# Performance work log

Hardware: AMD Instinct MI355X
Metric: run time of the kernel (lower is better)

## Reference

```python
import jax, jax.numpy as jnp
import numpy as np

EMBED = 1024
HEADS = 16


def setup_inputs() -> dict:
    key = jax.random.key(0)
    ks = jax.random.split(key, 7)
    scale = 1.0 / np.sqrt(EMBED)
    x = jax.random.normal(ks[0], (4, 2048, EMBED), dtype=jnp.float32)
    Wq = jax.random.normal(ks[1], (EMBED, EMBED), dtype=jnp.float32) * scale
    bq = jax.random.normal(ks[2], (EMBED,), dtype=jnp.float32) * 0.01
    Wk = jax.random.normal(ks[3], (EMBED, EMBED), dtype=jnp.float32) * scale
    bk = jax.random.normal(ks[4], (EMBED,), dtype=jnp.float32) * 0.01
    Wv = jax.random.normal(ks[5], (EMBED, EMBED), dtype=jnp.float32) * scale
    bv = jax.random.normal(ks[6], (EMBED,), dtype=jnp.float32) * 0.01
    return {"x": x, "Wq": Wq, "bq": bq, "Wk": Wk, "bk": bk, "Wv": Wv, "bv": bv}


def reference(x, Wq, bq, Wk, bk, Wv, bv):
    b, s, n = x.shape
    h = HEADS
    d = n // h
    # torch nn.Linear: y = x @ W.T + b
    q = (jnp.einsum("bsn,mn->bsm", x, Wq) + bq).reshape(b, s, h, d).transpose(0, 2, 1, 3)
    k = (jnp.einsum("bsn,mn->bsm", x, Wk) + bk).reshape(b, s, h, d).transpose(0, 2, 1, 3)
    v = (jnp.einsum("bsn,mn->bsm", x, Wv) + bv).reshape(b, s, h, d).transpose(0, 2, 1, 3)
    # scores: [b, h, s_q, s_k]; fixed scale of 1/10 as in the source
    scores = jnp.einsum("bhqd,bhkd->bhqk", q, k) / 10.0
    # NOTE: softmax over dim=-2 (the QUERY axis), matching the source exactly
    attn = jax.nn.softmax(scores, axis=-2)
    out = jnp.einsum("bhqk,bhkd->bhqd", attn, v)
    return out.transpose(0, 2, 1, 3).reshape(b, s, n)
```

## Files before the change

kernel.cpp:

```cpp
#include <hip/hip_runtime.h>
#include <math.h>

#define SEQ    2048
#define EMBED  1024
#define HEADS  16
#define HDIM   64
#define BATCH  4
#define ROWS   (BATCH * SEQ)
#define BH     (BATCH * HEADS)
#define NT     (SEQ / 64)

typedef _Float16 f16;
typedef __attribute__((ext_vector_type(8))) _Float16 f16x8;
typedef __attribute__((ext_vector_type(4))) _Float16 f16x4;
typedef __attribute__((ext_vector_type(4))) float    f32x4;

#define LOG2E_10 0.14426950408889634f

__device__ __forceinline__ float fast_exp2(float x) { return __builtin_amdgcn_exp2f(x); }

#define WAIT_VM0() asm volatile("s_waitcnt vmcnt(0)" ::: "memory")
#define WAIT_VM2() asm volatile("s_waitcnt vmcnt(2)" ::: "memory")
#define WAIT_VM4() asm volatile("s_waitcnt vmcnt(4)" ::: "memory")
#define WAIT_LGKM0() asm volatile("s_waitcnt lgkmcnt(0)" ::: "memory")
#define BAR() __builtin_amdgcn_s_barrier()

__device__ __forceinline__ void async16(void* l, const void* g) {
    __builtin_amdgcn_global_load_lds(
        (__attribute__((address_space(1))) void*)(uintptr_t)g,
        (__attribute__((address_space(3))) void*)(uint32_t)(uintptr_t)l,
        16, 0, 0);
}

__device__ __forceinline__ f32x4 mfma16(f16x8 a, f16x8 b, f32x4 c) {
    return __builtin_amdgcn_mfma_f32_16x16x32_f16(a, b, c, 0, 0, 0);
}
__device__ __forceinline__ f32x4 mfma16k16(f16x4 a, f16x4 b, f32x4 c) {
    return __builtin_amdgcn_mfma_f32_16x16x16f16(a, b, c, 0, 0, 0);
}

#define NX4 (ROWS * EMBED / 4)
#define NW4 (EMBED * EMBED / 4)
__global__ __launch_bounds__(256) void cvt_kernel(
    const float* __restrict__ x,
    const float* __restrict__ Wq, const float* __restrict__ Wk,
    const float* __restrict__ Wv,
    f16* __restrict__ xh, f16* __restrict__ Wh)
{
    int i = blockIdx.x * 256 + threadIdx.x;
    const float4* src; f16* dst; int j;
    if (i < NX4)              { src = (const float4*)x;  dst = xh;                j = i; }
    else if (i < NX4 + NW4)   { src = (const float4*)Wq; dst = Wh;                j = i - NX4; }
    else if (i < NX4 + 2*NW4) { src = (const float4*)Wk; dst = Wh + EMBED*EMBED;  j = i - NX4 - NW4; }
    else                      { src = (const float4*)Wv; dst = Wh + 2*EMBED*EMBED;j = i - NX4 - 2*NW4; }
    float4 v = src[j];
    f16x4 h;
    h[0] = (f16)v.x; h[1] = (f16)v.y; h[2] = (f16)v.z; h[3] = (f16)v.w;
    *(f16x4*)(dst + (size_t)j * 4) = h;
}

__global__ __launch_bounds__(256) void proj_kernel(
    const f16* __restrict__ A,
    const f16* __restrict__ W,
    const float* __restrict__ bq, const float* __restrict__ bk,
    const float* __restrict__ bv,
    f16* __restrict__ Qh, f16* __restrict__ Kh, f16* __restrict__ Vt)
{
    __shared__ f16 As[128 * 32];
    __shared__ f16 Bs[128 * 32];

    const int t = threadIdx.x, wv = t >> 6, lane = t & 63;
    const int lm = lane & 15, quad = lane >> 4;
    const int r0 = blockIdx.x * 128, c0 = blockIdx.y * 128;
    const int wm = wv & 1, wn = wv >> 1;

    const int srow = wv * 32 + (lane >> 2);
    const int sch  = (lane & 3) * 8;
    const f16* gA = A + (size_t)(r0 + srow) * EMBED + sch;
    const f16* gB = W + (size_t)(c0 + srow) * EMBED + sch;
    f16* lA = As + wv * 1024;
    f16* lB = Bs + wv * 1024;

    f32x4 acc[4][4];
#pragma unroll
    for (int i = 0; i < 4; ++i)
#pragma unroll
        for (int j = 0; j < 4; ++j) acc[i][j] = (f32x4){0.f, 0.f, 0.f, 0.f};

    for (int kk = 0; kk < EMBED; kk += 32) {
        __syncthreads();
        async16(lA,        gA + kk);
        async16(lA + 512,  gA + 16 * EMBED + kk);
        async16(lB,        gB + kk);
        async16(lB + 512,  gB + 16 * EMBED + kk);
        __syncthreads();

        f16x8 af[4], bf[4];
#pragma unroll
        for (int i = 0; i < 4; ++i)
            af[i] = *(const f16x8*)&As[(wm * 64 + i * 16 + lm) * 32 + quad * 8];
#pragma unroll
        for (int i = 0; i < 4; ++i)
            bf[i] = *(const f16x8*)&Bs[(wn * 64 + i * 16 + lm) * 32 + quad * 8];
#pragma unroll
        for (int mi = 0; mi < 4; ++mi)
#pragma unroll
            for (int ni = 0; ni < 4; ++ni)
                acc[mi][ni] = mfma16(af[mi], bf[ni], acc[mi][ni]);
    }

    const int z = c0 >> 10;
    const float* bias = (z == 0) ? bq : (z == 1) ? bk : bv;
    const float osc = (z == 0) ? LOG2E_10 : 1.0f;
#pragma unroll
    for (int ni = 0; ni < 4; ++ni) {
        int col = c0 + wn * 64 + ni * 16 + lm;
        int cz  = col & 1023;
        float bb = bias[cz];
        int h = cz >> 6, d = cz & 63;
#pragma unroll
        for (int mi = 0; mi < 4; ++mi) {
            int rbase = r0 + wm * 64 + mi * 16 + quad * 4;
            int b = rbase >> 11, s = rbase & 2047;
            if (z < 2) {
                f16* O = (z == 0) ? Qh : Kh;
                size_t base = ((size_t)(b * HEADS + h) * SEQ + s) * HDIM + d;
#pragma unroll
                for (int r = 0; r < 4; ++r)
                    O[base + (size_t)r * HDIM] = (f16)((acc[mi][ni][r] + bb) * osc);
            } else {
                f16x4 pk;
#pragma unroll
                for (int r = 0; r < 4; ++r) pk[r] = (f16)(acc[mi][ni][r] + bb);
                *(f16x4*)&Vt[((size_t)(b * HEADS + h) * HDIM + d) * SEQ + s] = pk;
            }
        }
    }
}

__device__ __forceinline__ void xcd_decode(int d, int& bh, int& x128) {
    int xcd  = d & 7;
    int r    = d >> 3;
    x128     = (r & 15) * 128;
    bh       = (r >> 4) * 8 + xcd;
}

__global__ __launch_bounds__(256) void stats_kernel(
    const f16* __restrict__ Qh, const f16* __restrict__ Kh,
    const f16* __restrict__ Vt, f16* __restrict__ Vt2)
{
    __shared__ f16 Ks[128 * 64];
    __shared__ f16 Qs[2 * 64 * 64];

    const int t = threadIdx.x, wv = t >> 6, lane = t & 63;
    const int lm = lane & 15, quad = lane >> 4;
    int bh, k0;
    xcd_decode(blockIdx.x, bh, k0);
    const int grow = lane >> 3;
    const int gsw  = ((lane & 7) ^ grow) * 8;
    const int rs   = lm & 7;
    const size_t base = (size_t)bh * SEQ * HDIM;

#pragma unroll
    for (int i = 0; i < 4; ++i) {
        int g = wv * 4 + i;
        async16(Ks + g * 512, Kh + base + (size_t)(k0 + g * 8 + grow) * HDIM + gsw);
    }
#pragma unroll
    for (int bi = 0; bi < 2; ++bi)
#pragma unroll
        for (int i = 0; i < 2; ++i) {
            int g = wv * 2 + i;
            async16(Qs + bi * 4096 + g * 512,
                    Qh + base + (size_t)(bi * 64 + g * 8 + grow) * HDIM + gsw);
        }
    WAIT_VM4();
    BAR();

    f16x8 kf[2][2];
#pragma unroll
    for (int ct = 0; ct < 2; ++ct)
#pragma unroll
        for (int ds = 0; ds < 2; ++ds)
            kf[ct][ds] = *(const f16x8*)&Ks[(wv * 32 + ct * 16 + lm) * 64
                                            + (((ds * 4 + quad) ^ rs) << 3)];

    float cs0 = 0.f, cs1 = 0.f;
    for (int it = 0; it < NT; ++it) {
        const int cur = it & 1;
        if (it == NT - 1) WAIT_VM0(); else WAIT_VM2();
        BAR();
        const f16* Qb = Qs + cur * 4096;
#pragma unroll
        for (int qt = 0; qt < 4; ++qt) {
            f16x8 a0 = *(const f16x8*)&Qb[(qt * 16 + lm) * 64 + ((quad ^ rs) << 3)];
            f16x8 a1 = *(const f16x8*)&Qb[(qt * 16 + lm) * 64 + (((4 + quad) ^ rs) << 3)];
            f32x4 c0v = (f32x4){0.f, 0.f, 0.f, 0.f};
            f32x4 c1v = (f32x4){0.f, 0.f, 0.f, 0.f};
            c0v = mfma16(a0, kf[0][0], c0v); c0v = mfma16(a1, kf[0][1], c0v);
            c1v = mfma16(a0, kf[1][0], c1v); c1v = mfma16(a1, kf[1][1], c1v);
#pragma unroll
            for (int r = 0; r < 4; ++r) {
                cs0 += fast_exp2(c0v[r]);
                cs1 += fast_exp2(c1v[r]);
            }
        }
        WAIT_LGKM0();
        BAR();
        if (it + 2 < NT) {
            const int qn = (it + 2) * 64;
#pragma unroll
            for (int i = 0; i < 2; ++i) {
                int g = wv * 2 + i;
                async16(Qs + cur * 4096 + g * 512,
                        Qh + base + (size_t)(qn + g * 8 + grow) * HDIM + gsw);
            }
        }
    }
    cs0 += __shfl_xor(cs0, 16, 64); cs0 += __shfl_xor(cs0, 32, 64);
    cs1 += __shfl_xor(cs1, 16, 64); cs1 += __shfl_xor(cs1, 32, 64);

    float* sc = (float*)Qs;
    if (quad == 0) {
        sc[wv * 32 + lm]      = 1024.0f / cs0;
        sc[wv * 32 + 16 + lm] = 1024.0f / cs1;
    }
    __syncthreads();
    const int row = t >> 2, cb = (t & 3) * 32;
    const f16* src = Vt  + base + (size_t)row * SEQ + k0 + cb;
    f16*       dst = Vt2 + base + (size_t)row * SEQ + k0 + cb;
#pragma unroll
    for (int c = 0; c < 4; ++c) {
        f16x8 v = *(const f16x8*)(src + c * 8);
        f16x8 o;
#pragma unroll
        for (int j = 0; j < 8; ++j)
            o[j] = (f16)((float)v[j] * sc[cb + c * 8 + j]);
        *(f16x8*)(dst + c * 8) = o;
    }
}

__global__ __launch_bounds__(256) void out_kernel(
    const f16* __restrict__ Qh, const f16* __restrict__ Kh,
    const f16* __restrict__ Vt2, float* __restrict__ out)
{
    __shared__ f16 L[16384];

    const int t = threadIdx.x, wv = t >> 6, lane = t & 63;
    const int lm = lane & 15, quad = lane >> 4;
    const int wq = wv >> 1, wk = wv & 1;
    int bh, q0;
    xcd_decode(blockIdx.x, bh, q0);
    const int b = bh >> 4, h = bh & 15;
    const int grow = lane >> 3;
    const int gsw  = ((lane & 7) ^ grow) * 8;
    const int rs   = lm & 7;
    const size_t base = (size_t)bh * SEQ * HDIM;

#pragma unroll
    for (int i = 0; i < 4; ++i) {
        int g = wv * 4 + i;
        async16(L + g * 512, Qh + base + (size_t)(q0 + g * 8 + grow) * HDIM + gsw);
    }
    WAIT_VM0();
    BAR();
    f16x8 qa[4][2];
#pragma unroll
    for (int qt = 0; qt < 4; ++qt)
#pragma unroll
        for (int ds = 0; ds < 2; ++ds)
            qa[qt][ds] = *(const f16x8*)&L[(wq * 64 + qt * 16 + lm) * 64
                                           + (((ds * 4 + quad) ^ rs) << 3)];
    WAIT_LGKM0();
    BAR();
#pragma unroll
    for (int bi = 0; bi < 2; ++bi)
#pragma unroll
        for (int i = 0; i < 2; ++i) {
            int g = wv * 2 + i;
            async16(L + bi * 4096 + g * 512,
                    Kh + base + (size_t)(bi * 64 + g * 8 + grow) * HDIM + gsw);
            async16(L + 8192 + bi * 4096 + g * 512,
                    Vt2 + base + (size_t)(g * 8 + grow) * SEQ + bi * 64 + gsw);
        }

    f32x4 oacc[4][4];
#pragma unroll
    for (int i = 0; i < 4; ++i)
#pragma unroll
        for (int j = 0; j < 4; ++j) oacc[i][j] = (f32x4){0.f, 0.f, 0.f, 0.f};

    for (int it = 0; it < NT; ++it) {
        const int cur = it & 1;
        if (it == NT - 1) WAIT_VM0(); else WAIT_VM4();
        BAR();
        const f16* Kb = L + cur * 4096;
        const f16* Vb = L + 8192 + cur * 4096;

#pragma unroll
        for (int ct = 0; ct < 2; ++ct) {
            const int kb = wk * 32 + ct * 16;
            f16x8 kf0 = *(const f16x8*)&Kb[(kb + lm) * 64 + ((quad ^ rs) << 3)];
            f16x8 kf1 = *(const f16x8*)&Kb[(kb + lm) * 64 + (((4 + quad) ^ rs) << 3)];
            const int vch = ((wk * 4 + ct * 2 + (quad >> 1)) ^ rs);
            f16x4 vb[4];
#pragma unroll
            for (int dt = 0; dt < 4; ++dt)
                vb[dt] = *(const f16x4*)&Vb[(dt * 16 + lm) * 64 + vch * 8 + (quad & 1) * 4];
#pragma unroll
            for (int qt = 0; qt < 4; ++qt) {
                f32x4 s4 = (f32x4){0.f, 0.f, 0.f, 0.f};
                s4 = mfma16(kf0, qa[qt][0], s4);
                s4 = mfma16(kf1, qa[qt][1], s4);
                f16x4 pa;
#pragma unroll
                for (int r = 0; r < 4; ++r)
                    pa[r] = (f16)fast_exp2(s4[r]);
#pragma unroll
                for (int dt = 0; dt < 4; ++dt)
                    oacc[qt][dt] = mfma16k16(pa, vb[dt], oacc[qt][dt]);
            }
        }
        WAIT_LGKM0();
        BAR();
        if (it + 2 < NT) {
            const int kn = (it + 2) * 64;
#pragma unroll
            for (int i = 0; i < 2; ++i) {
                int g = wv * 2 + i;
                async16(L + cur * 4096 + g * 512,
                        Kh + base + (size_t)(kn + g * 8 + grow) * HDIM + gsw);
                async16(L + 8192 + cur * 4096 + g * 512,
                        Vt2 + base + (size_t)(g * 8 + grow) * SEQ + kn + gsw);
            }
        }
    }

    float* red = (float*)L;
    if (wk == 1) {
#pragma unroll
        for (int qt = 0; qt < 4; ++qt)
#pragma unroll
            for (int dt = 0; dt < 4; ++dt)
#pragma unroll
                for (int r = 0; r < 4; ++r)
                    red[wq * 4096 + (qt * 16 + quad * 4 + r) * 64 + dt * 16 + lm]
                        = oacc[qt][dt][r];
    }
    __syncthreads();
    if (wk == 0) {
        const float inv1024 = 1.0f / 1024.0f;
#pragma unroll
        for (int qt = 0; qt < 4; ++qt)
#pragma unroll
            for (int dt = 0; dt < 4; ++dt) {
                int col = h * HDIM + dt * 16 + lm;
#pragma unroll
                for (int r = 0; r < 4; ++r) {
                    int ql = qt * 16 + quad * 4 + r;
                    int s  = q0 + wq * 64 + ql;
                    float v = oacc[qt][dt][r]
                            + red[wq * 4096 + ql * 64 + dt * 16 + lm];
                    out[((size_t)b * SEQ + s) * EMBED + col] = v * inv1024;
                }
            }
    }
}

extern "C" void kernel_launch(void* const* d_in, const int* in_sizes, int n_in,
                              void* d_out, int out_size, void* d_ws, size_t ws_size,
                              hipStream_t stream) {
    const float* x  = (const float*)d_in[0];
    const float* Wq = (const float*)d_in[1];
    const float* bq = (const float*)d_in[2];
    const float* Wk = (const float*)d_in[3];
    const float* bk = (const float*)d_in[4];
    const float* Wv = (const float*)d_in[5];
    const float* bv = (const float*)d_in[6];
    float* out = (float*)d_out;

    f16* xh = (f16*)d_ws;
    f16* Wh = xh + (size_t)ROWS * EMBED;
    f16* Qh = Wh + (size_t)3 * EMBED * EMBED;
    f16* Kh = Qh + (size_t)BH * SEQ * HDIM;
    f16* Vt = Kh + (size_t)BH * SEQ * HDIM;
    f16* Vt2 = xh;

    cvt_kernel<<<(NX4 + 3 * NW4) / 256, 256, 0, stream>>>(x, Wq, Wk, Wv, xh, Wh);
    proj_kernel<<<dim3(ROWS / 128, 3 * EMBED / 128), 256, 0, stream>>>(
        xh, Wh, bq, bk, bv, Qh, Kh, Vt);
    stats_kernel<<<dim3(SEQ / 128 * BH), 256, 0, stream>>>(Qh, Kh, Vt, Vt2);
    out_kernel<<<dim3(SEQ / 128 * BH), 256, 0, stream>>>(Qh, Kh, Vt2, out);
}
```

Before: 307.0 us.

## Restructure projection GEMM with 256x128 tiles, triple-buffered async LDS pipeline

The QKV projection GEMM now uses 512-thread blocks computing 256x128 tiles with a 64-wide K step. A three-slot dynamic shared-memory ring is filled by async global-to-LDS loads issued two steps ahead, and the tiles use an XOR-swizzled layout to avoid bank conflicts. Each K step is split into two MFMA halves with s_setprio raised around the math so loads overlap compute. This targets the per-iteration load/sync stalls of the old single-buffered 32-wide loop. In exchange it uses much more LDS (one block per CU), needs a dynamic shared memory attribute, and depends on fragile manual vmcnt accounting.

```diff
diff --git a/kernel.cpp b/kernel.cpp
--- a/kernel.cpp
+++ b/kernel.cpp
@@ -9,6 +9,8 @@
 #define ROWS   (BATCH * SEQ)
 #define BH     (BATCH * HEADS)
 #define NT     (SEQ / 64)
+#define NKT    16
+#define PSLOT  24576
 
 typedef _Float16 f16;
 typedef __attribute__((ext_vector_type(8))) _Float16 f16x8;
@@ -20,8 +22,8 @@
 __device__ __forceinline__ float fast_exp2(float x) { return __builtin_amdgcn_exp2f(x); }
 
 #define WAIT_VM0() asm volatile("s_waitcnt vmcnt(0)" ::: "memory")
-#define WAIT_VM2() asm volatile("s_waitcnt vmcnt(2)" ::: "memory")
 #define WAIT_VM4() asm volatile("s_waitcnt vmcnt(4)" ::: "memory")
+#define WAIT_VM6() asm volatile("s_waitcnt vmcnt(6)" ::: "memory")
 #define WAIT_LGKM0() asm volatile("s_waitcnt lgkmcnt(0)" ::: "memory")
 #define BAR() __builtin_amdgcn_s_barrier()
 
@@ -59,68 +61,125 @@
     *(f16x4*)(dst + (size_t)j * 4) = h;
 }
 
-__global__ __launch_bounds__(256) void proj_kernel(
+__global__ __launch_bounds__(512, 1) void proj_kernel(
     const f16* __restrict__ A,
     const f16* __restrict__ W,
     const float* __restrict__ bq, const float* __restrict__ bk,
     const float* __restrict__ bv,
     f16* __restrict__ Qh, f16* __restrict__ Kh, f16* __restrict__ Vt)
 {
-    __shared__ f16 As[128 * 32];
-    __shared__ f16 Bs[128 * 32];
+    extern __shared__ f16 Ls[];
 
     const int t = threadIdx.x, wv = t >> 6, lane = t & 63;
     const int lm = lane & 15, quad = lane >> 4;
-    const int r0 = blockIdx.x * 128, c0 = blockIdx.y * 128;
     const int wm = wv & 1, wn = wv >> 1;
-
-    const int srow = wv * 32 + (lane >> 2);
-    const int sch  = (lane & 3) * 8;
-    const f16* gA = A + (size_t)(r0 + srow) * EMBED + sch;
-    const f16* gB = W + (size_t)(c0 + srow) * EMBED + sch;
-    f16* lA = As + wv * 1024;
-    f16* lB = Bs + wv * 1024;
-
-    f32x4 acc[4][4];
-#pragma unroll
-    for (int i = 0; i < 4; ++i)
-#pragma unroll
-        for (int j = 0; j < 4; ++j) acc[i][j] = (f32x4){0.f, 0.f, 0.f, 0.f};
-
-    for (int kk = 0; kk < EMBED; kk += 32) {
-        __syncthreads();
-        async16(lA,        gA + kk);
-        async16(lA + 512,  gA + 16 * EMBED + kk);
-        async16(lB,        gB + kk);
-        async16(lB + 512,  gB + 16 * EMBED + kk);
-        __syncthreads();
-
-        f16x8 af[4], bf[4];
-#pragma unroll
-        for (int i = 0; i < 4; ++i)
-            af[i] = *(const f16x8*)&As[(wm * 64 + i * 16 + lm) * 32 + quad * 8];
-#pragma unroll
-        for (int i = 0; i < 4; ++i)
-            bf[i] = *(const f16x8*)&Bs[(wn * 64 + i * 16 + lm) * 32 + quad * 8];
+    const int r0 = blockIdx.x * 256, c0 = blockIdx.y * 128;
+    const int grow = lane >> 3;
+    const int gsw  = ((lane & 7) ^ grow) * 8;
+    const int rs   = lm & 7;
+
+    f32x4 acc[8][2];
+#pragma unroll
+    for (int i = 0; i < 8; ++i)
+#pragma unroll
+        for (int j = 0; j < 2; ++j) acc[i][j] = (f32x4){0.f, 0.f, 0.f, 0.f};
+
+#pragma unroll
+    for (int tt = 0; tt < 2; ++tt) {
+#pragma unroll
+        for (int j = 0; j < 4; ++j)
+            async16(Ls + tt * PSLOT + (j * 64 + wv * 8) * 64,
+                    A + (size_t)(r0 + j * 64 + wv * 8 + grow) * EMBED + tt * 64 + gsw);
+#pragma unroll
+        for (int j = 0; j < 2; ++j)
+            async16(Ls + tt * PSLOT + 16384 + (j * 64 + wv * 8) * 64,
+                    W + (size_t)(c0 + j * 64 + wv * 8 + grow) * EMBED + tt * 64 + gsw);
+    }
+    WAIT_VM6();
+    BAR();
+
+    int sl = 0;
+    for (int kt = 0; kt < NKT; ++kt) {
+        const f16* Ab = Ls + sl * PSLOT;
+        const f16* Bb = Ab + 16384;
+        const int ns = (sl == 0) ? 2 : sl - 1;
+        const int kn = (kt + 2) * 64;
+
+        f16x8 af[4][2], bf[2][2];
 #pragma unroll
         for (int mi = 0; mi < 4; ++mi)
 #pragma unroll
-            for (int ni = 0; ni < 4; ++ni)
-                acc[mi][ni] = mfma16(af[mi], bf[ni], acc[mi][ni]);
+            for (int kk = 0; kk < 2; ++kk)
+                af[mi][kk] = *(const f16x8*)&Ab[(wm * 128 + mi * 16 + lm) * 64
+                                                + (((kk * 4 + quad) ^ rs) << 3)];
+#pragma unroll
+        for (int ni = 0; ni < 2; ++ni)
+#pragma unroll
+            for (int kk = 0; kk < 2; ++kk)
+                bf[ni][kk] = *(const f16x8*)&Bb[(wn * 32 + ni * 16 + lm) * 64
+                                                + (((kk * 4 + quad) ^ rs) << 3)];
+        if (kt + 2 < NKT) {
+#pragma unroll
+            for (int j = 0; j < 4; ++j)
+                async16(Ls + ns * PSLOT + (j * 64 + wv * 8) * 64,
+                        A + (size_t)(r0 + j * 64 + wv * 8 + grow) * EMBED + kn + gsw);
+        }
+        BAR();
+        WAIT_LGKM0();
+        __builtin_amdgcn_s_setprio(1);
+#pragma unroll
+        for (int mi = 0; mi < 4; ++mi)
+#pragma unroll
+            for (int ni = 0; ni < 2; ++ni) {
+                acc[mi][ni] = mfma16(af[mi][0], bf[ni][0], acc[mi][ni]);
+                acc[mi][ni] = mfma16(af[mi][1], bf[ni][1], acc[mi][ni]);
+            }
+        __builtin_amdgcn_s_setprio(0);
+        BAR();
+
+#pragma unroll
+        for (int mi = 0; mi < 4; ++mi)
+#pragma unroll
+            for (int kk = 0; kk < 2; ++kk)
+                af[mi][kk] = *(const f16x8*)&Ab[(wm * 128 + (mi + 4) * 16 + lm) * 64
+                                                + (((kk * 4 + quad) ^ rs) << 3)];
+        if (kt + 2 < NKT) {
+#pragma unroll
+            for (int j = 0; j < 2; ++j)
+                async16(Ls + ns * PSLOT + 16384 + (j * 64 + wv * 8) * 64,
+                        W + (size_t)(c0 + j * 64 + wv * 8 + grow) * EMBED + kn + gsw);
+            WAIT_VM6();
+        } else {
+            WAIT_VM0();
+        }
+        BAR();
+        WAIT_LGKM0();
+        __builtin_amdgcn_s_setprio(1);
+#pragma unroll
+        for (int mi = 0; mi < 4; ++mi)
+#pragma unroll
+            for (int ni = 0; ni < 2; ++ni) {
+                acc[mi + 4][ni] = mfma16(af[mi][0], bf[ni][0], acc[mi + 4][ni]);
+                acc[mi + 4][ni] = mfma16(af[mi][1], bf[ni][1], acc[mi + 4][ni]);
+            }
+        __builtin_amdgcn_s_setprio(0);
+        BAR();
+
+        sl = (sl == 2) ? 0 : sl + 1;
     }
 
     const int z = c0 >> 10;
     const float* bias = (z == 0) ? bq : (z == 1) ? bk : bv;
     const float osc = (z == 0) ? LOG2E_10 : 1.0f;
 #pragma unroll
-    for (int ni = 0; ni < 4; ++ni) {
-        int col = c0 + wn * 64 + ni * 16 + lm;
+    for (int ni = 0; ni < 2; ++ni) {
+        int col = c0 + wn * 32 + ni * 16 + lm;
         int cz  = col & 1023;
         float bb = bias[cz];
         int h = cz >> 6, d = cz & 63;
 #pragma unroll
-        for (int mi = 0; mi < 4; ++mi) {
-            int rbase = r0 + wm * 64 + mi * 16 + quad * 4;
+        for (int mi = 0; mi < 8; ++mi) {
+            int rbase = r0 + wm * 128 + mi * 16 + quad * 4;
             int b = rbase >> 11, s = rbase & 2047;
             if (z < 2) {
                 f16* O = (z == 0) ? Qh : Kh;
@@ -188,7 +247,8 @@
     float cs0 = 0.f, cs1 = 0.f;
     for (int it = 0; it < NT; ++it) {
         const int cur = it & 1;
-        if (it == NT - 1) WAIT_VM0(); else WAIT_VM2();
+        if (it == NT - 1) WAIT_VM0();
+        else asm volatile("s_waitcnt vmcnt(2)" ::: "memory");
         BAR();
         const f16* Qb = Qs + cur * 4096;
 #pragma unroll
@@ -386,8 +446,17 @@
     f16* Vt = Kh + (size_t)BH * SEQ * HDIM;
     f16* Vt2 = xh;
 
+    static int attr_set = 0;
+    if (!attr_set) {
+        hipFuncSetAttribute((const void*)proj_kernel,
+                            hipFuncAttributeMaxDynamicSharedMemorySize,
+                            3 * PSLOT * (int)sizeof(f16));
+        attr_set = 1;
+    }
+
     cvt_kernel<<<(NX4 + 3 * NW4) / 256, 256, 0, stream>>>(x, Wq, Wk, Wv, xh, Wh);
-    proj_kernel<<<dim3(ROWS / 128, 3 * EMBED / 128), 256, 0, stream>>>(
+    proj_kernel<<<dim3(ROWS / 256, 3 * EMBED / 128), 512,
+                  3 * PSLOT * sizeof(f16), stream>>>(
         xh, Wh, bq, bk, bv, Qh, Kh, Vt);
     stats_kernel<<<dim3(SEQ / 128 * BH), 256, 0, stream>>>(Qh, Kh, Vt, Vt2);
     out_kernel<<<dim3(SEQ / 128 * BH), 256, 0, stream>>>(Qh, Kh, Vt2, out);
```

After: 310.5 us. About the same (+1.1%).

## Apply column-softmax scale to probabilities in out_kernel instead of rescaling V

Applied to the files above, without the earlier changes.

The stats kernel no longer rewrites a scaled copy of V; it writes only the per-key reciprocal column sums to a small float buffer. The output kernel stages all 2048 scale factors for its head in LDS using 4-byte async loads and multiplies each exp2 result by its key's scale before the PV MFMA. This removes a full read and write pass over V. The cost is an extra multiply per probability and more LDS in out_kernel. s_setprio is also raised around the MFMA sections of both kernels.

```diff
diff --git a/kernel.cpp b/kernel.cpp
--- a/kernel.cpp
+++ b/kernel.cpp
@@ -30,6 +30,12 @@
         (__attribute__((address_space(1))) void*)(uintptr_t)g,
         (__attribute__((address_space(3))) void*)(uint32_t)(uintptr_t)l,
         16, 0, 0);
+}
+__device__ __forceinline__ void async4(void* l, const void* g) {
+    __builtin_amdgcn_global_load_lds(
+        (__attribute__((address_space(1))) void*)(uintptr_t)g,
+        (__attribute__((address_space(3))) void*)(uint32_t)(uintptr_t)l,
+        4, 0, 0);
 }
 
 __device__ __forceinline__ f32x4 mfma16(f16x8 a, f16x8 b, f32x4 c) {
@@ -147,7 +153,7 @@
 
 __global__ __launch_bounds__(256) void stats_kernel(
     const f16* __restrict__ Qh, const f16* __restrict__ Kh,
-    const f16* __restrict__ Vt, f16* __restrict__ Vt2)
+    float* __restrict__ scv)
 {
     __shared__ f16 Ks[128 * 64];
     __shared__ f16 Qs[2 * 64 * 64];
@@ -191,6 +197,7 @@
         if (it == NT - 1) WAIT_VM0(); else WAIT_VM2();
         BAR();
         const f16* Qb = Qs + cur * 4096;
+        __builtin_amdgcn_s_setprio(1);
 #pragma unroll
         for (int qt = 0; qt < 4; ++qt) {
             f16x8 a0 = *(const f16x8*)&Qb[(qt * 16 + lm) * 64 + ((quad ^ rs) << 3)];
@@ -205,6 +212,7 @@
                 cs1 += fast_exp2(c1v[r]);
             }
         }
+        __builtin_amdgcn_s_setprio(0);
         WAIT_LGKM0();
         BAR();
         if (it + 2 < NT) {
@@ -219,32 +227,18 @@
     }
     cs0 += __shfl_xor(cs0, 16, 64); cs0 += __shfl_xor(cs0, 32, 64);
     cs1 += __shfl_xor(cs1, 16, 64); cs1 += __shfl_xor(cs1, 32, 64);
-
-    float* sc = (float*)Qs;
     if (quad == 0) {
-        sc[wv * 32 + lm]      = 1024.0f / cs0;
-        sc[wv * 32 + 16 + lm] = 1024.0f / cs1;
-    }
-    __syncthreads();
-    const int row = t >> 2, cb = (t & 3) * 32;
-    const f16* src = Vt  + base + (size_t)row * SEQ + k0 + cb;
-    f16*       dst = Vt2 + base + (size_t)row * SEQ + k0 + cb;
-#pragma unroll
-    for (int c = 0; c < 4; ++c) {
-        f16x8 v = *(const f16x8*)(src + c * 8);
-        f16x8 o;
-#pragma unroll
-        for (int j = 0; j < 8; ++j)
-            o[j] = (f16)((float)v[j] * sc[cb + c * 8 + j]);
-        *(f16x8*)(dst + c * 8) = o;
+        scv[(size_t)bh * SEQ + k0 + wv * 32 + lm]      = 1024.0f / cs0;
+        scv[(size_t)bh * SEQ + k0 + wv * 32 + 16 + lm] = 1024.0f / cs1;
     }
 }
 
 __global__ __launch_bounds__(256) void out_kernel(
     const f16* __restrict__ Qh, const f16* __restrict__ Kh,
-    const f16* __restrict__ Vt2, float* __restrict__ out)
+    const f16* __restrict__ Vt, const float* __restrict__ scv,
+    float* __restrict__ out)
 {
-    __shared__ f16 L[16384];
+    __shared__ f16 L[20480];
 
     const int t = threadIdx.x, wv = t >> 6, lane = t & 63;
     const int lm = lane & 15, quad = lane >> 4;
@@ -257,6 +251,8 @@
     const int rs   = lm & 7;
     const size_t base = (size_t)bh * SEQ * HDIM;
 
+    float* scf = (float*)(L + 16384);
+
 #pragma unroll
     for (int i = 0; i < 4; ++i) {
         int g = wv * 4 + i;
@@ -274,6 +270,10 @@
     WAIT_LGKM0();
     BAR();
 #pragma unroll
+    for (int c = 0; c < 8; ++c)
+        async4(scf + c * 256 + wv * 64,
+               scv + (size_t)bh * SEQ + c * 256 + wv * 64 + lane);
+#pragma unroll
     for (int bi = 0; bi < 2; ++bi)
 #pragma unroll
         for (int i = 0; i < 2; ++i) {
@@ -281,7 +281,7 @@
             async16(L + bi * 4096 + g * 512,
                     Kh + base + (size_t)(bi * 64 + g * 8 + grow) * HDIM + gsw);
             async16(L + 8192 + bi * 4096 + g * 512,
-                    Vt2 + base + (size_t)(g * 8 + grow) * SEQ + bi * 64 + gsw);
+                    Vt + base + (size_t)(g * 8 + grow) * SEQ + bi * 64 + gsw);
         }
 
     f32x4 oacc[4][4];
@@ -296,12 +296,15 @@
         BAR();
         const f16* Kb = L + cur * 4096;
         const f16* Vb = L + 8192 + cur * 4096;
-
+        const float* scb = scf + it * 64;
+
+        __builtin_amdgcn_s_setprio(1);
 #pragma unroll
         for (int ct = 0; ct < 2; ++ct) {
             const int kb = wk * 32 + ct * 16;
             f16x8 kf0 = *(const f16x8*)&Kb[(kb + lm) * 64 + ((quad ^ rs) << 3)];
             f16x8 kf1 = *(const f16x8*)&Kb[(kb + lm) * 64 + (((4 + quad) ^ rs) << 3)];
+            f32x4 sc4 = *(const f32x4*)&scb[kb + quad * 4];
             const int vch = ((wk * 4 + ct * 2 + (quad >> 1)) ^ rs);
             f16x4 vb[4];
 #pragma unroll
@@ -315,12 +318,13 @@
                 f16x4 pa;
 #pragma unroll
                 for (int r = 0; r < 4; ++r)
-                    pa[r] = (f16)fast_exp2(s4[r]);
+                    pa[r] = (f16)(fast_exp2(s4[r]) * sc4[r]);
 #pragma unroll
                 for (int dt = 0; dt < 4; ++dt)
                     oacc[qt][dt] = mfma16k16(pa, vb[dt], oacc[qt][dt]);
             }
         }
+        __builtin_amdgcn_s_setprio(0);
         WAIT_LGKM0();
         BAR();
         if (it + 2 < NT) {
@@ -331,7 +335,7 @@
                 async16(L + cur * 4096 + g * 512,
                         Kh + base + (size_t)(kn + g * 8 + grow) * HDIM + gsw);
                 async16(L + 8192 + cur * 4096 + g * 512,
-                        Vt2 + base + (size_t)(g * 8 + grow) * SEQ + kn + gsw);
+                        Vt + base + (size_t)(g * 8 + grow) * SEQ + kn + gsw);
             }
         }
     }
@@ -384,11 +388,11 @@
     f16* Qh = Wh + (size_t)3 * EMBED * EMBED;
     f16* Kh = Qh + (size_t)BH * SEQ * HDIM;
     f16* Vt = Kh + (size_t)BH * SEQ * HDIM;
-    f16* Vt2 = xh;
+    float* scv = (float*)(Vt + (size_t)BH * SEQ * HDIM);
 
     cvt_kernel<<<(NX4 + 3 * NW4) / 256, 256, 0, stream>>>(x, Wq, Wk, Wv, xh, Wh);
     proj_kernel<<<dim3(ROWS / 128, 3 * EMBED / 128), 256, 0, stream>>>(
         xh, Wh, bq, bk, bv, Qh, Kh, Vt);
-    stats_kernel<<<dim3(SEQ / 128 * BH), 256, 0, stream>>>(Qh, Kh, Vt, Vt2);
-    out_kernel<<<dim3(SEQ / 128 * BH), 256, 0, stream>>>(Qh, Kh, Vt2, out);
-}
+    stats_kernel<<<dim3(SEQ / 128 * BH), 256, 0, stream>>>(Qh, Kh, scv);
+    out_kernel<<<dim3(SEQ / 128 * BH), 256, 0, stream>>>(Qh, Kh, Vt, scv, out);
+}
```

Result: no change. 310.0 us (+1.0%).
